# Performance work log

Measured on AMD Instinct MI355X. Metric: run time of the kernel, lower is better.

## Reference

```python
import jax, jax.numpy as jnp
import numpy as np

NEG_SLOPE = 0.2

def leaky_relu(x):
    return jnp.where(x >= 0, x, NEG_SLOPE * x)

def conv1x1(x, w, b):
    # x: [n,c,h,w], w: [o,c], b: [o]
    return jnp.einsum('nchw,oc->nohw', x, w) + b[None, :, None, None]

def setup_inputs() -> dict:
    key = jax.random.key(0)
    ks = jax.random.split(key, 7)
    n, c, h, w = 4, 64, 80, 80
    scale = 1.0 / np.sqrt(c)
    return {
        'x': jax.random.normal(ks[0], (n, c, h, w), dtype=jnp.float32),
        'w1': jax.random.normal(ks[1], (c, c), dtype=jnp.float32) * scale,
        'b1': jax.random.normal(ks[2], (c,), dtype=jnp.float32) * 0.01,
        'w2': jax.random.normal(ks[3], (c, c), dtype=jnp.float32) * scale,
        'b2': jax.random.normal(ks[4], (c,), dtype=jnp.float32) * 0.01,
        'w3': jax.random.normal(ks[5], (c, c), dtype=jnp.float32) * scale,
        'b3': jax.random.normal(ks[6], (c,), dtype=jnp.float32) * 0.01,
    }

def reference(x, w1, b1, w2, b2, w3, b3):
    n, c, h, w = x.shape
    e1 = leaky_relu(conv1x1(x, w1, b1))  # [n,c,h,w]
    e2 = leaky_relu(conv1x1(x, w2, b2))
    asm = leaky_relu(conv1x1(x, w3, b3))
    # q: [n, hw, c]; k: [n, c, hw]
    q = e1.transpose(0, 2, 3, 1).reshape(n, h * w, c)
    k = e2.reshape(n, c, h * w)
    score = jax.nn.softmax(jnp.matmul(q, k), axis=2)  # [n, hw, hw]
    v = asm.reshape(n, c, h * w).transpose(0, 2, 1)   # [n, hw, c]
    out = jnp.matmul(score, v)                        # [n, hw, c]
    return out.transpose(0, 2, 1).reshape(n, c, h, w)
```

## Files before the change

kernel.cpp:

```cpp
#include <hip/hip_runtime.h>


typedef __attribute__((ext_vector_type(8))) unsigned short us8;
typedef __attribute__((ext_vector_type(4))) unsigned short us4;
typedef __attribute__((ext_vector_type(8))) __bf16 bf16x8;
typedef __attribute__((ext_vector_type(16))) float f32x16;

#define HW 6400
#define L2E 1.44269504088896340736f
#define KS 5
#define ITERS 20

union V8 { us8 s; us4 h[2]; bf16x8 b; unsigned u4[4]; };

__device__ __forceinline__ unsigned short f32_to_bf16(float f) {
  unsigned u = __float_as_uint(f);
  u += 0x7fffu + ((u >> 16) & 1u);
  return (unsigned short)(u >> 16);
}
__device__ __forceinline__ float bf16_bits_to_f32(unsigned short u) {
  return __uint_as_float(((unsigned)u) << 16);
}
__device__ __forceinline__ unsigned pack_bf16x2(float a, float b) {
#if __has_builtin(__builtin_amdgcn_cvt_pk_bf16_f32)
  auto v = __builtin_amdgcn_cvt_pk_bf16_f32(a, b);
  unsigned u;
  __builtin_memcpy(&u, &v, 4);
  return u;
#else
  unsigned ua = __float_as_uint(a); ua += 0x7fffu + ((ua >> 16) & 1u);
  unsigned ub = __float_as_uint(b); ub += 0x7fffu + ((ub >> 16) & 1u);
  return (ua >> 16) | (ub & 0xffff0000u);
#endif
}

__global__ __launch_bounds__(256) void wprep_kernel(
    const float* __restrict__ w1, const float* __restrict__ b1,
    const float* __restrict__ w2, const float* __restrict__ w3,
    unsigned short* __restrict__ Whl, float* __restrict__ b1s) {
  const int tid = blockIdx.x * 256 + threadIdx.x;
  if (tid < 3 * 4096) {
    const int k = tid >> 12;
    const int rem = tid & 4095;
    const float* wsrc = (k == 0) ? w1 : (k == 1) ? w2 : w3;
    float v = wsrc[rem];
    if (k == 0) v *= L2E;
    const unsigned short hi = f32_to_bf16(v);
    const unsigned short lo = f32_to_bf16(v - bf16_bits_to_f32(hi));
    Whl[(size_t)(k * 2) * 4096 + rem] = hi;
    Whl[(size_t)(k * 2 + 1) * 4096 + rem] = lo;
  }
  if (tid < 64) b1s[tid] = b1[tid] * L2E;
}

__global__ __launch_bounds__(256, 2) void conv_kernel(
    const float* __restrict__ x, const unsigned short* __restrict__ Whl,
    const float* __restrict__ b1s, const float* __restrict__ b2,
    const float* __restrict__ b3,
    unsigned short* __restrict__ Qg, unsigned short* __restrict__ Kg,
    unsigned short* __restrict__ Vg) {
  __shared__ __align__(16) unsigned short Xh[64 * 72];
  __shared__ __align__(16) unsigned short Xl[64 * 72];
  __shared__ __align__(16) unsigned short tb[64 * 72];

  const int t = threadIdx.x;
  const int n = blockIdx.y;
  const int p0 = blockIdx.x * 64;
  const int wv = t >> 6;
  const int lane = t & 63;
  const int l31 = lane & 31;
  const int lh = lane >> 5;
  const int ob = (wv & 1) * 32;
  const int pw = (wv >> 1) * 32;

  {
    const int c2 = t >> 3;
    const int pg = (t & 7) * 8;
    const float* s0 = x + ((size_t)(n * 64 + 2 * c2) * HW + p0 + pg);
    const float* s1 = s0 + HW;
    float a0[8], a1[8];
    *(float4*)(a0) = *(const float4*)s0;
    *(float4*)(a0 + 4) = *(const float4*)(s0 + 4);
    *(float4*)(a1) = *(const float4*)s1;
    *(float4*)(a1 + 4) = *(const float4*)(s1 + 4);
#pragma unroll
    for (int j = 0; j < 8; ++j) {
      const unsigned hp = pack_bf16x2(a0[j], a1[j]);
      const float r0 = a0[j] - bf16_bits_to_f32((unsigned short)(hp & 0xffffu));
      const float r1 = a1[j] - bf16_bits_to_f32((unsigned short)(hp >> 16));
      const unsigned lq = pack_bf16x2(r0, r1);
      ((unsigned*)Xh)[(pg + j) * 36 + c2] = hp;
      ((unsigned*)Xl)[(pg + j) * 36 + c2] = lq;
    }
  }
  __syncthreads();

#pragma unroll 1
  for (int k = 0; k < 3; ++k) {
    const unsigned short* Wh = Whl + (size_t)(k * 2) * 4096;
    const unsigned short* Wl = Wh + 4096;
    const float* bm = (k == 0) ? b1s : (k == 1) ? b2 : b3;

    V8 ah[4], al[4];
#pragma unroll
    for (int kst = 0; kst < 4; ++kst) {
      const int off = (ob + l31) * 64 + kst * 16 + lh * 8;
      ah[kst].s = *(const us8*)(Wh + off);
      al[kst].s = *(const us8*)(Wl + off);
    }

    f32x16 acc;
#pragma unroll
    for (int r = 0; r < 16; ++r) acc[r] = 0.f;

#pragma unroll
    for (int kst = 0; kst < 4; ++kst) {
      V8 bh, bl;
      const int xoff = (pw + l31) * 72 + kst * 16 + lh * 8;
      bh.s = *(const us8*)(Xh + xoff);
      bl.s = *(const us8*)(Xl + xoff);
      acc = __builtin_amdgcn_mfma_f32_32x32x16_bf16(al[kst].b, bh.b, acc, 0, 0, 0);
      acc = __builtin_amdgcn_mfma_f32_32x32x16_bf16(ah[kst].b, bl.b, acc, 0, 0, 0);
      acc = __builtin_amdgcn_mfma_f32_32x32x16_bf16(ah[kst].b, bh.b, acc, 0, 0, 0);
    }

    if (k < 2) {
#pragma unroll
      for (int rq = 0; rq < 4; ++rq) {
        const int o = ob + 8 * rq + 4 * lh;
        const int pcol = pw + l31;
        float v[4];
#pragma unroll
        for (int j = 0; j < 4; ++j) {
          float a = acc[4 * rq + j] + bm[o + j];
          a = fmaxf(a, 0.f) + 0.2f * fminf(a, 0.f);
          v[j] = a;
        }
        unsigned* dst = (unsigned*)(tb + pcol * 72 + o);
        dst[0] = pack_bf16x2(v[0], v[1]);
        dst[1] = pack_bf16x2(v[2], v[3]);
      }
      __syncthreads();
      {
        const int p = t >> 2, part = t & 3;
        const unsigned short* src = tb + p * 72 + part * 16;
        unsigned short* dst = (k == 0 ? Qg : Kg) +
                              (size_t)(n * HW + p0 + p) * 64 + part * 16;
        *(us8*)dst = *(const us8*)src;
        *(us8*)(dst + 8) = *(const us8*)(src + 8);
      }
      __syncthreads();
    } else {
#pragma unroll
      for (int r = 0; r < 16; ++r) {
        const int o = ob + 8 * (r >> 2) + 4 * lh + (r & 3);
        const int pcol = pw + l31;
        float a = acc[r] + bm[o];
        a = fmaxf(a, 0.f) + 0.2f * fminf(a, 0.f);
        Vg[(size_t)(n * 64 + o) * HW + p0 + pcol] = f32_to_bf16(a);
      }
    }
  }
}

__global__ __launch_bounds__(256, 4) void attn_kernel(
    const unsigned short* __restrict__ Qg, const unsigned short* __restrict__ Kg,
    const unsigned short* __restrict__ Vg, unsigned short* __restrict__ Opart,
    float* __restrict__ Lpart) {
  __shared__ __align__(16) char smem[36864];
  unsigned short* Otb = (unsigned short*)smem;

  const int t = threadIdx.x;
  const int w = t >> 6;
  const int lane = t & 63;
  const int l31 = lane & 31;
  const int lh = lane >> 5;
  const int nb = blockIdx.y;
  const int qb = blockIdx.x * 128;
  const int ks = blockIdx.z;
  const int key0 = ks * (HW / KS);

  V8 aQ[4];
  {
    const unsigned short* qrow =
        Qg + (size_t)(nb * HW + qb + w * 32 + l31) * 64 + lh * 8;
#pragma unroll
    for (int kst = 0; kst < 4; ++kst) aQ[kst].s = *(const us8*)(qrow + kst * 16);
  }

  f32x16 accO[2];
#pragma unroll
  for (int ci = 0; ci < 2; ++ci)
#pragma unroll
    for (int r = 0; r < 16; ++r) accO[ci][r] = 0.f;
  float lp = 0.f;

  f32x16 zero16;
#pragma unroll
  for (int r = 0; r < 16; ++r) zero16[r] = 0.f;

  const int soff = (t >> 2) * 72 + (t & 3) * 16;
  const unsigned short* ksrc =
      Kg + (size_t)nb * HW * 64 + (size_t)(key0 + (t >> 2)) * 64 + (t & 3) * 16;
  const unsigned short* vsrc =
      Vg + (size_t)nb * 64 * HW + (size_t)(t >> 2) * HW + key0 + (t & 3) * 16;

  V8 kr0, kr1, vr0, vr1;
  kr0.s = *(const us8*)ksrc;
  kr1.s = *(const us8*)(ksrc + 8);
  vr0.s = *(const us8*)vsrc;
  vr1.s = *(const us8*)(vsrc + 8);
  {
    unsigned short* kd = (unsigned short*)smem + soff;
    unsigned short* vd = (unsigned short*)(smem + 18432) + soff;
    *(us8*)kd = kr0.s; *(us8*)(kd + 8) = kr1.s;
    *(us8*)vd = vr0.s; *(us8*)(vd + 8) = vr1.s;
  }
  __syncthreads();

#pragma unroll 1
  for (int jt = 0; jt < ITERS; ++jt) {
    const int b = jt & 1;
    const unsigned short* Kc = (const unsigned short*)(smem + b * 9216);
    const unsigned short* Vc = (const unsigned short*)(smem + 18432 + b * 9216);
    const bool more = (jt + 1 < ITERS);

    if (more) {
      kr0.s = *(const us8*)(ksrc + (jt + 1) * 4096);
      kr1.s = *(const us8*)(ksrc + (jt + 1) * 4096 + 8);
      vr0.s = *(const us8*)(vsrc + (jt + 1) * 64);
      vr1.s = *(const us8*)(vsrc + (jt + 1) * 64 + 8);
    }

#pragma unroll
    for (int ni = 0; ni < 2; ++ni) {
      V8 ak[4];
#pragma unroll
      for (int kst = 0; kst < 4; ++kst)
        ak[kst].s = *(const us8*)(Kc + (ni * 32 + l31) * 72 + kst * 16 + lh * 8);
      f32x16 sacc =
          __builtin_amdgcn_mfma_f32_32x32x16_bf16(ak[0].b, aQ[0].b, zero16, 0, 0, 0);
#pragma unroll
      for (int kst = 1; kst < 4; ++kst)
        sacc = __builtin_amdgcn_mfma_f32_32x32x16_bf16(ak[kst].b, aQ[kst].b,
                                                       sacc, 0, 0, 0);
      uint2 pkg[4];
#pragma unroll
      for (int g = 0; g < 4; ++g) {
        const float p0 = __builtin_amdgcn_exp2f(sacc[4 * g + 0]);
        const float p1 = __builtin_amdgcn_exp2f(sacc[4 * g + 1]);
        const float p2 = __builtin_amdgcn_exp2f(sacc[4 * g + 2]);
        const float p3 = __builtin_amdgcn_exp2f(sacc[4 * g + 3]);
        lp += (p0 + p1) + (p2 + p3);
        pkg[g].x = pack_bf16x2(p0, p1);
        pkg[g].y = pack_bf16x2(p2, p3);
      }

      V8 bv[2][2];
#pragma unroll
      for (int ci = 0; ci < 2; ++ci)
#pragma unroll
        for (int kk = 0; kk < 2; ++kk)
          bv[ci][kk].s = *(const us8*)(Vc + (ci * 32 + l31) * 72 +
                                       (2 * ni + kk) * 16 + lh * 8);
#pragma unroll
      for (int kk = 0; kk < 2; ++kk) {
        const int gb = 2 * kk;
        V8 ap;
#if __has_builtin(__builtin_amdgcn_permlane32_swap)
        {
          auto rx = __builtin_amdgcn_permlane32_swap(pkg[gb].x, pkg[gb + 1].x,
                                                     false, false);
          auto ry = __builtin_amdgcn_permlane32_swap(pkg[gb].y, pkg[gb + 1].y,
                                                     false, false);
          ap.u4[0] = rx[0]; ap.u4[2] = rx[1];
          ap.u4[1] = ry[0]; ap.u4[3] = ry[1];
        }
#else
        {
          const uint2 qa = pkg[gb];
          const uint2 qb2 = pkg[gb + 1];
          uint2 send;
          send.x = lh ? qa.x : qb2.x;
          send.y = lh ? qa.y : qb2.y;
          uint2 recv;
          recv.x = __shfl_xor(send.x, 32);
          recv.y = __shfl_xor(send.y, 32);
          const uint2 keep = {lh ? qb2.x : qa.x, lh ? qb2.y : qa.y};
          ap.u4[0] = lh ? recv.x : keep.x;
          ap.u4[1] = lh ? recv.y : keep.y;
          ap.u4[2] = lh ? keep.x : recv.x;
          ap.u4[3] = lh ? keep.y : recv.y;
        }
#endif
        accO[0] = __builtin_amdgcn_mfma_f32_32x32x16_bf16(ap.b, bv[0][kk].b,
                                                          accO[0], 0, 0, 0);
        accO[1] = __builtin_amdgcn_mfma_f32_32x32x16_bf16(ap.b, bv[1][kk].b,
                                                          accO[1], 0, 0, 0);
      }
    }

    if (more) {
      unsigned short* kd = (unsigned short*)(smem + (1 - b) * 9216) + soff;
      unsigned short* vd = (unsigned short*)(smem + 18432 + (1 - b) * 9216) + soff;
      *(us8*)kd = kr0.s; *(us8*)(kd + 8) = kr1.s;
      *(us8*)vd = vr0.s; *(us8*)(vd + 8) = vr1.s;
      __syncthreads();
    }
  }

  {
    const float lsum = lp + __shfl_xor(lp, 32);
    if (lh == 0)
      Lpart[((size_t)ks * 4 + nb) * HW + qb + w * 32 + l31] = lsum;
  }

  __syncthreads();
#pragma unroll
  for (int ci = 0; ci < 2; ++ci)
#pragma unroll
    for (int r = 0; r < 16; ++r) {
      const int qcol = w * 32 + 8 * (r >> 2) + 4 * lh + (r & 3);
      Otb[(ci * 32 + l31) * 132 + qcol] = f32_to_bf16(accO[ci][r]);
    }
  __syncthreads();
  {
    const int ch = t >> 2, part = t & 3;
    const unsigned short* src = Otb + ch * 132 + part * 32;
    unsigned short* dst =
        Opart + (((size_t)ks * 4 + nb) * 64 + ch) * HW + qb + part * 32;
#pragma unroll
    for (int i = 0; i < 4; ++i) {
      V8 v;
      v.h[0] = *(const us4*)(src + i * 8);
      v.h[1] = *(const us4*)(src + i * 8 + 4);
      *(us8*)(dst + i * 8) = v.s;
    }
  }
}

__global__ __launch_bounds__(256) void combine_kernel(
    const unsigned short* __restrict__ Opart, const float* __restrict__ Lpart,
    float* __restrict__ out) {
  const int tid = blockIdx.x * 256 + threadIdx.x;
  const size_t e = (size_t)tid * 4;
  float4 o = {0.f, 0.f, 0.f, 0.f};
#pragma unroll
  for (int ks = 0; ks < KS; ++ks) {
    const us4 v = *(const us4*)(Opart + (size_t)ks * (4 * 64 * HW) + e);
    o.x += bf16_bits_to_f32(v[0]);
    o.y += bf16_bits_to_f32(v[1]);
    o.z += bf16_bits_to_f32(v[2]);
    o.w += bf16_bits_to_f32(v[3]);
  }
  const int n = (int)(e / (64 * HW));
  const int p = (int)(e % HW);
  float4 l = {0.f, 0.f, 0.f, 0.f};
#pragma unroll
  for (int ks = 0; ks < KS; ++ks) {
    const float4 v = *(const float4*)(Lpart + ((size_t)ks * 4 + n) * HW + p);
    l.x += v.x; l.y += v.y; l.z += v.z; l.w += v.w;
  }
  float4 r;
  r.x = o.x / l.x; r.y = o.y / l.y; r.z = o.z / l.z; r.w = o.w / l.w;
  *(float4*)(out + e) = r;
}

extern "C" void kernel_launch(void* const* d_in, const int* in_sizes, int n_in,
                              void* d_out, int out_size, void* d_ws, size_t ws_size,
                              hipStream_t stream) {
  const float* x = (const float*)d_in[0];
  const float* w1 = (const float*)d_in[1];
  const float* b1 = (const float*)d_in[2];
  const float* w2 = (const float*)d_in[3];
  const float* b2 = (const float*)d_in[4];
  const float* w3 = (const float*)d_in[5];
  const float* b3 = (const float*)d_in[6];
  float* out = (float*)d_out;

  unsigned short* Q = (unsigned short*)d_ws;
  unsigned short* K = Q + (size_t)4 * HW * 64;
  unsigned short* V = K + (size_t)4 * HW * 64;
  unsigned short* Opart = V + (size_t)4 * HW * 64;
  float* Lpart = (float*)(Opart + (size_t)KS * 4 * 64 * HW);
  unsigned short* Whl = (unsigned short*)(Lpart + (size_t)KS * 4 * HW);
  float* b1s = (float*)(Whl + 3 * 2 * 4096);

  wprep_kernel<<<48, 256, 0, stream>>>(w1, b1, w2, w3, Whl, b1s);
  conv_kernel<<<dim3(100, 4), 256, 0, stream>>>(x, Whl, b1s, b2, b3, Q, K, V);
  attn_kernel<<<dim3(50, 4, KS), 256, 0, stream>>>(Q, K, V, Opart, Lpart);
  combine_kernel<<<1600, 256, 0, stream>>>(Opart, Lpart, out);
}
```

Before: 145.3 us.

## Fuse split-K combine into attention kernel via last-block atomic counter

Removes the separate combine kernel. Each attention block bumps a per-tile atomic counter once its partial output is written, and the last of the KS key-split blocks sums the bf16 partials and the L partials, then writes the normalized output. This saves one kernel launch and lets the combine overlap with attention blocks still running, at the cost of a threadfence and an atomic per block and a serialized reduction tail in the last block. The counters are reset inside wprep on every call.

```diff
diff --git a/kernel.cpp b/kernel.cpp
--- a/kernel.cpp
+++ b/kernel.cpp
@@ -37,7 +37,8 @@
 __global__ __launch_bounds__(256) void wprep_kernel(
     const float* __restrict__ w1, const float* __restrict__ b1,
     const float* __restrict__ w2, const float* __restrict__ w3,
-    unsigned short* __restrict__ Whl, float* __restrict__ b1s) {
+    unsigned short* __restrict__ Whl, float* __restrict__ b1s,
+    int* __restrict__ cnt) {
   const int tid = blockIdx.x * 256 + threadIdx.x;
   if (tid < 3 * 4096) {
     const int k = tid >> 12;
@@ -51,6 +52,7 @@
     Whl[(size_t)(k * 2 + 1) * 4096 + rem] = lo;
   }
   if (tid < 64) b1s[tid] = b1[tid] * L2E;
+  if (tid < 200) cnt[tid] = 0;
 }
 
 __global__ __launch_bounds__(256, 2) void conv_kernel(
@@ -166,7 +168,8 @@
 __global__ __launch_bounds__(256, 4) void attn_kernel(
     const unsigned short* __restrict__ Qg, const unsigned short* __restrict__ Kg,
     const unsigned short* __restrict__ Vg, unsigned short* __restrict__ Opart,
-    float* __restrict__ Lpart) {
+    float* __restrict__ Lpart, int* __restrict__ cnt,
+    float* __restrict__ out) {
   __shared__ __align__(16) char smem[36864];
   unsigned short* Otb = (unsigned short*)smem;
 
@@ -337,33 +340,60 @@
       *(us8*)(dst + i * 8) = v.s;
     }
   }
-}
-
-__global__ __launch_bounds__(256) void combine_kernel(
-    const unsigned short* __restrict__ Opart, const float* __restrict__ Lpart,
-    float* __restrict__ out) {
-  const int tid = blockIdx.x * 256 + threadIdx.x;
-  const size_t e = (size_t)tid * 4;
-  float4 o = {0.f, 0.f, 0.f, 0.f};
-#pragma unroll
-  for (int ks = 0; ks < KS; ++ks) {
-    const us4 v = *(const us4*)(Opart + (size_t)ks * (4 * 64 * HW) + e);
-    o.x += bf16_bits_to_f32(v[0]);
-    o.y += bf16_bits_to_f32(v[1]);
-    o.z += bf16_bits_to_f32(v[2]);
-    o.w += bf16_bits_to_f32(v[3]);
-  }
-  const int n = (int)(e / (64 * HW));
-  const int p = (int)(e % HW);
-  float4 l = {0.f, 0.f, 0.f, 0.f};
-#pragma unroll
-  for (int ks = 0; ks < KS; ++ks) {
-    const float4 v = *(const float4*)(Lpart + ((size_t)ks * 4 + n) * HW + p);
-    l.x += v.x; l.y += v.y; l.z += v.z; l.w += v.w;
-  }
-  float4 r;
-  r.x = o.x / l.x; r.y = o.y / l.y; r.z = o.z / l.z; r.w = o.w / l.w;
-  *(float4*)(out + e) = r;
+
+  __threadfence();
+  __syncthreads();
+  __shared__ int lastflag;
+  if (t == 0) {
+    const int old = __hip_atomic_fetch_add(&cnt[nb * 50 + blockIdx.x], 1,
+                                           __ATOMIC_ACQ_REL,
+                                           __HIP_MEMORY_SCOPE_AGENT);
+    lastflag = (old == KS - 1);
+  }
+  __syncthreads();
+  if (!lastflag) return;
+  __threadfence();
+
+  {
+    const int c = t >> 2;
+    const int pseg = (t & 3) * 32;
+#pragma unroll
+    for (int hhalf = 0; hhalf < 2; ++hhalf) {
+      const int pb2 = pseg + hhalf * 16;
+      float osum[16], lsum[16];
+#pragma unroll
+      for (int j = 0; j < 16; ++j) { osum[j] = 0.f; lsum[j] = 0.f; }
+#pragma unroll
+      for (int ksi = 0; ksi < KS; ++ksi) {
+        const unsigned short* op =
+            Opart + (((size_t)ksi * 4 + nb) * 64 + c) * HW + qb + pb2;
+        const us8 v0 = *(const us8*)op;
+        const us8 v1 = *(const us8*)(op + 8);
+#pragma unroll
+        for (int j = 0; j < 8; ++j) {
+          osum[j] += bf16_bits_to_f32(v0[j]);
+          osum[8 + j] += bf16_bits_to_f32(v1[j]);
+        }
+        const float* lptr = Lpart + ((size_t)ksi * 4 + nb) * HW + qb + pb2;
+#pragma unroll
+        for (int j = 0; j < 4; ++j) {
+          const float4 lv = *(const float4*)(lptr + j * 4);
+          lsum[4 * j + 0] += lv.x; lsum[4 * j + 1] += lv.y;
+          lsum[4 * j + 2] += lv.z; lsum[4 * j + 3] += lv.w;
+        }
+      }
+      float* od = out + ((size_t)nb * 64 + c) * HW + qb + pb2;
+#pragma unroll
+      for (int j = 0; j < 4; ++j) {
+        float4 r;
+        r.x = osum[4 * j + 0] / lsum[4 * j + 0];
+        r.y = osum[4 * j + 1] / lsum[4 * j + 1];
+        r.z = osum[4 * j + 2] / lsum[4 * j + 2];
+        r.w = osum[4 * j + 3] / lsum[4 * j + 3];
+        *(float4*)(od + j * 4) = r;
+      }
+    }
+  }
 }
 
 extern "C" void kernel_launch(void* const* d_in, const int* in_sizes, int n_in,
@@ -385,9 +415,10 @@
   float* Lpart = (float*)(Opart + (size_t)KS * 4 * 64 * HW);
   unsigned short* Whl = (unsigned short*)(Lpart + (size_t)KS * 4 * HW);
   float* b1s = (float*)(Whl + 3 * 2 * 4096);
-
-  wprep_kernel<<<48, 256, 0, stream>>>(w1, b1, w2, w3, Whl, b1s);
+  int* cnt = (int*)(b1s + 64);
+
+  wprep_kernel<<<48, 256, 0, stream>>>(w1, b1, w2, w3, Whl, b1s, cnt);
   conv_kernel<<<dim3(100, 4), 256, 0, stream>>>(x, Whl, b1s, b2, b3, Q, K, V);
-  attn_kernel<<<dim3(50, 4, KS), 256, 0, stream>>>(Q, K, V, Opart, Lpart);
-  combine_kernel<<<1600, 256, 0, stream>>>(Opart, Lpart, out);
-}
+  attn_kernel<<<dim3(50, 4, KS), 256, 0, stream>>>(Q, K, V, Opart, Lpart,
+                                                   cnt, out);
+}
```

New measurement: 334.0 us. 130% more time.

## Load K/V tiles directly from global into registers, drop LDS double-buffering

Applied to the files above, without the earlier changes.

Removes the shared-memory double-buffered staging of K and V tiles and their per-iteration barriers. Each wave now loads its MFMA operands straight from global memory (via L2/cache) into registers, with the loop unrolled by two. Occupancy bounds drop from 4 to 3 blocks to allow more registers. This trades fewer syncs and LDS traffic for redundant global loads, since all four waves fetch the same K/V, plus exposed global latency and reduced occupancy.

```diff
diff --git a/kernel.cpp b/kernel.cpp
--- a/kernel.cpp
+++ b/kernel.cpp
@@ -163,12 +163,11 @@
   }
 }
 
-__global__ __launch_bounds__(256, 4) void attn_kernel(
+__global__ __launch_bounds__(256, 3) void attn_kernel(
     const unsigned short* __restrict__ Qg, const unsigned short* __restrict__ Kg,
     const unsigned short* __restrict__ Vg, unsigned short* __restrict__ Opart,
     float* __restrict__ Lpart) {
-  __shared__ __align__(16) char smem[36864];
-  unsigned short* Otb = (unsigned short*)smem;
+  __shared__ __align__(16) unsigned short Otb[64 * 132];
 
   const int t = threadIdx.x;
   const int w = t >> 6;
@@ -199,45 +198,35 @@
 #pragma unroll
   for (int r = 0; r < 16; ++r) zero16[r] = 0.f;
 
-  const int soff = (t >> 2) * 72 + (t & 3) * 16;
-  const unsigned short* ksrc =
-      Kg + (size_t)nb * HW * 64 + (size_t)(key0 + (t >> 2)) * 64 + (t & 3) * 16;
-  const unsigned short* vsrc =
-      Vg + (size_t)nb * 64 * HW + (size_t)(t >> 2) * HW + key0 + (t & 3) * 16;
-
-  V8 kr0, kr1, vr0, vr1;
-  kr0.s = *(const us8*)ksrc;
-  kr1.s = *(const us8*)(ksrc + 8);
-  vr0.s = *(const us8*)vsrc;
-  vr1.s = *(const us8*)(vsrc + 8);
-  {
-    unsigned short* kd = (unsigned short*)smem + soff;
-    unsigned short* vd = (unsigned short*)(smem + 18432) + soff;
-    *(us8*)kd = kr0.s; *(us8*)(kd + 8) = kr1.s;
-    *(us8*)vd = vr0.s; *(us8*)(vd + 8) = vr1.s;
-  }
-  __syncthreads();
-
-#pragma unroll 1
+  const unsigned short* Kw = Kg + ((size_t)nb * HW + key0) * 64;
+  const unsigned short* Vw = Vg + (size_t)nb * 64 * HW + key0;
+
+#pragma unroll 2
   for (int jt = 0; jt < ITERS; ++jt) {
-    const int b = jt & 1;
-    const unsigned short* Kc = (const unsigned short*)(smem + b * 9216);
-    const unsigned short* Vc = (const unsigned short*)(smem + 18432 + b * 9216);
-    const bool more = (jt + 1 < ITERS);
-
-    if (more) {
-      kr0.s = *(const us8*)(ksrc + (jt + 1) * 4096);
-      kr1.s = *(const us8*)(ksrc + (jt + 1) * 4096 + 8);
-      vr0.s = *(const us8*)(vsrc + (jt + 1) * 64);
-      vr1.s = *(const us8*)(vsrc + (jt + 1) * 64 + 8);
-    }
+    const int kb = jt * 64;
+
+    V8 ak0[4], ak1[4];
+#pragma unroll
+    for (int kst = 0; kst < 4; ++kst) {
+      ak0[kst].s = *(const us8*)(Kw + (size_t)(kb + l31) * 64 + kst * 16 + lh * 8);
+      ak1[kst].s =
+          *(const us8*)(Kw + (size_t)(kb + 32 + l31) * 64 + kst * 16 + lh * 8);
+    }
+    V8 bv0[2][2], bv1[2][2];
+#pragma unroll
+    for (int ci = 0; ci < 2; ++ci)
+#pragma unroll
+      for (int kk = 0; kk < 2; ++kk) {
+        const unsigned short* vrow = Vw + (size_t)(ci * 32 + l31) * HW + kb;
+        bv0[ci][kk].s = *(const us8*)(vrow + kk * 16 + lh * 8);
+        bv1[ci][kk].s = *(const us8*)(vrow + 32 + kk * 16 + lh * 8);
+      }
 
 #pragma unroll
     for (int ni = 0; ni < 2; ++ni) {
-      V8 ak[4];
-#pragma unroll
-      for (int kst = 0; kst < 4; ++kst)
-        ak[kst].s = *(const us8*)(Kc + (ni * 32 + l31) * 72 + kst * 16 + lh * 8);
+      V8* ak = ni ? ak1 : ak0;
+      V8(*bv)[2] = ni ? bv1 : bv0;
+
       f32x16 sacc =
           __builtin_amdgcn_mfma_f32_32x32x16_bf16(ak[0].b, aQ[0].b, zero16, 0, 0, 0);
 #pragma unroll
@@ -256,13 +245,6 @@
         pkg[g].y = pack_bf16x2(p2, p3);
       }
 
-      V8 bv[2][2];
-#pragma unroll
-      for (int ci = 0; ci < 2; ++ci)
-#pragma unroll
-        for (int kk = 0; kk < 2; ++kk)
-          bv[ci][kk].s = *(const us8*)(Vc + (ci * 32 + l31) * 72 +
-                                       (2 * ni + kk) * 16 + lh * 8);
 #pragma unroll
       for (int kk = 0; kk < 2; ++kk) {
         const int gb = 2 * kk;
@@ -299,14 +281,6 @@
                                                           accO[1], 0, 0, 0);
       }
     }
-
-    if (more) {
-      unsigned short* kd = (unsigned short*)(smem + (1 - b) * 9216) + soff;
-      unsigned short* vd = (unsigned short*)(smem + 18432 + (1 - b) * 9216) + soff;
-      *(us8*)kd = kr0.s; *(us8*)(kd + 8) = kr1.s;
-      *(us8*)vd = vr0.s; *(us8*)(vd + 8) = vr1.s;
-      __syncthreads();
-    }
   }
 
   {
@@ -315,7 +289,6 @@
       Lpart[((size_t)ks * 4 + nb) * HW + qb + w * 32 + l31] = lsum;
   }
 
-  __syncthreads();
 #pragma unroll
   for (int ci = 0; ci < 2; ++ci)
 #pragma unroll
```

Result: slower. 245.4 us (+68.9%).

## Process two query tiles per wave to reuse K/V LDS fragments

Applied to the files above, without the earlier changes.

Each wave now handles 64 query rows (two 32-row MFMA tiles) instead of 32, so every K and V fragment loaded from shared memory feeds twice as many MFMAs. The attention grid is halved to 25x4x5 blocks and launch bounds drop to 2 blocks per CU to allow the larger register footprint. The output staging buffer is widened to a 266-element row stride. The trade-off is fewer blocks to spread over the CUs, lower occupancy, and potentially misaligned 8-byte shared loads from the new stride.

```diff
diff --git a/kernel.cpp b/kernel.cpp
--- a/kernel.cpp
+++ b/kernel.cpp
@@ -163,7 +163,7 @@
   }
 }
 
-__global__ __launch_bounds__(256, 4) void attn_kernel(
+__global__ __launch_bounds__(256, 2) void attn_kernel(
     const unsigned short* __restrict__ Qg, const unsigned short* __restrict__ Kg,
     const unsigned short* __restrict__ Vg, unsigned short* __restrict__ Opart,
     float* __restrict__ Lpart) {
@@ -176,24 +176,28 @@
   const int l31 = lane & 31;
   const int lh = lane >> 5;
   const int nb = blockIdx.y;
-  const int qb = blockIdx.x * 128;
+  const int qb = blockIdx.x * 256;
   const int ks = blockIdx.z;
   const int key0 = ks * (HW / KS);
 
-  V8 aQ[4];
-  {
+  V8 aQ[2][4];
+#pragma unroll
+  for (int h = 0; h < 2; ++h) {
     const unsigned short* qrow =
-        Qg + (size_t)(nb * HW + qb + w * 32 + l31) * 64 + lh * 8;
-#pragma unroll
-    for (int kst = 0; kst < 4; ++kst) aQ[kst].s = *(const us8*)(qrow + kst * 16);
-  }
-
-  f32x16 accO[2];
-#pragma unroll
-  for (int ci = 0; ci < 2; ++ci)
-#pragma unroll
-    for (int r = 0; r < 16; ++r) accO[ci][r] = 0.f;
-  float lp = 0.f;
+        Qg + (size_t)(nb * HW + qb + w * 64 + h * 32 + l31) * 64 + lh * 8;
+#pragma unroll
+    for (int kst = 0; kst < 4; ++kst)
+      aQ[h][kst].s = *(const us8*)(qrow + kst * 16);
+  }
+
+  f32x16 accO[2][2];
+#pragma unroll
+  for (int h = 0; h < 2; ++h)
+#pragma unroll
+    for (int ci = 0; ci < 2; ++ci)
+#pragma unroll
+      for (int r = 0; r < 16; ++r) accO[h][ci][r] = 0.f;
+  float lp0 = 0.f, lp1 = 0.f;
 
   f32x16 zero16;
 #pragma unroll
@@ -238,22 +242,29 @@
 #pragma unroll
       for (int kst = 0; kst < 4; ++kst)
         ak[kst].s = *(const us8*)(Kc + (ni * 32 + l31) * 72 + kst * 16 + lh * 8);
-      f32x16 sacc =
-          __builtin_amdgcn_mfma_f32_32x32x16_bf16(ak[0].b, aQ[0].b, zero16, 0, 0, 0);
-#pragma unroll
-      for (int kst = 1; kst < 4; ++kst)
-        sacc = __builtin_amdgcn_mfma_f32_32x32x16_bf16(ak[kst].b, aQ[kst].b,
-                                                       sacc, 0, 0, 0);
-      uint2 pkg[4];
-#pragma unroll
-      for (int g = 0; g < 4; ++g) {
-        const float p0 = __builtin_amdgcn_exp2f(sacc[4 * g + 0]);
-        const float p1 = __builtin_amdgcn_exp2f(sacc[4 * g + 1]);
-        const float p2 = __builtin_amdgcn_exp2f(sacc[4 * g + 2]);
-        const float p3 = __builtin_amdgcn_exp2f(sacc[4 * g + 3]);
-        lp += (p0 + p1) + (p2 + p3);
-        pkg[g].x = pack_bf16x2(p0, p1);
-        pkg[g].y = pack_bf16x2(p2, p3);
+
+      uint2 pkg[2][4];
+#pragma unroll
+      for (int h = 0; h < 2; ++h) {
+        f32x16 sacc = __builtin_amdgcn_mfma_f32_32x32x16_bf16(
+            ak[0].b, aQ[h][0].b, zero16, 0, 0, 0);
+#pragma unroll
+        for (int kst = 1; kst < 4; ++kst)
+          sacc = __builtin_amdgcn_mfma_f32_32x32x16_bf16(ak[kst].b,
+                                                         aQ[h][kst].b, sacc,
+                                                         0, 0, 0);
+        float lps = 0.f;
+#pragma unroll
+        for (int g = 0; g < 4; ++g) {
+          const float p0 = __builtin_amdgcn_exp2f(sacc[4 * g + 0]);
+          const float p1 = __builtin_amdgcn_exp2f(sacc[4 * g + 1]);
+          const float p2 = __builtin_amdgcn_exp2f(sacc[4 * g + 2]);
+          const float p3 = __builtin_amdgcn_exp2f(sacc[4 * g + 3]);
+          lps += (p0 + p1) + (p2 + p3);
+          pkg[h][g].x = pack_bf16x2(p0, p1);
+          pkg[h][g].y = pack_bf16x2(p2, p3);
+        }
+        if (h == 0) lp0 += lps; else lp1 += lps;
       }
 
       V8 bv[2][2];
@@ -263,40 +274,44 @@
         for (int kk = 0; kk < 2; ++kk)
           bv[ci][kk].s = *(const us8*)(Vc + (ci * 32 + l31) * 72 +
                                        (2 * ni + kk) * 16 + lh * 8);
+
 #pragma unroll
       for (int kk = 0; kk < 2; ++kk) {
         const int gb = 2 * kk;
-        V8 ap;
+#pragma unroll
+        for (int h = 0; h < 2; ++h) {
+          V8 ap;
 #if __has_builtin(__builtin_amdgcn_permlane32_swap)
-        {
-          auto rx = __builtin_amdgcn_permlane32_swap(pkg[gb].x, pkg[gb + 1].x,
-                                                     false, false);
-          auto ry = __builtin_amdgcn_permlane32_swap(pkg[gb].y, pkg[gb + 1].y,
-                                                     false, false);
-          ap.u4[0] = rx[0]; ap.u4[2] = rx[1];
-          ap.u4[1] = ry[0]; ap.u4[3] = ry[1];
+          {
+            auto rx = __builtin_amdgcn_permlane32_swap(
+                pkg[h][gb].x, pkg[h][gb + 1].x, false, false);
+            auto ry = __builtin_amdgcn_permlane32_swap(
+                pkg[h][gb].y, pkg[h][gb + 1].y, false, false);
+            ap.u4[0] = rx[0]; ap.u4[2] = rx[1];
+            ap.u4[1] = ry[0]; ap.u4[3] = ry[1];
+          }
+#else
+          {
+            const uint2 qa = pkg[h][gb];
+            const uint2 qb2 = pkg[h][gb + 1];
+            uint2 send;
+            send.x = lh ? qa.x : qb2.x;
+            send.y = lh ? qa.y : qb2.y;
+            uint2 recv;
+            recv.x = __shfl_xor(send.x, 32);
+            recv.y = __shfl_xor(send.y, 32);
+            const uint2 keep = {lh ? qb2.x : qa.x, lh ? qb2.y : qa.y};
+            ap.u4[0] = lh ? recv.x : keep.x;
+            ap.u4[1] = lh ? recv.y : keep.y;
+            ap.u4[2] = lh ? keep.x : recv.x;
+            ap.u4[3] = lh ? keep.y : recv.y;
+          }
+#endif
+          accO[h][0] = __builtin_amdgcn_mfma_f32_32x32x16_bf16(
+              ap.b, bv[0][kk].b, accO[h][0], 0, 0, 0);
+          accO[h][1] = __builtin_amdgcn_mfma_f32_32x32x16_bf16(
+              ap.b, bv[1][kk].b, accO[h][1], 0, 0, 0);
         }
-#else
-        {
-          const uint2 qa = pkg[gb];
-          const uint2 qb2 = pkg[gb + 1];
-          uint2 send;
-          send.x = lh ? qa.x : qb2.x;
-          send.y = lh ? qa.y : qb2.y;
-          uint2 recv;
-          recv.x = __shfl_xor(send.x, 32);
-          recv.y = __shfl_xor(send.y, 32);
-          const uint2 keep = {lh ? qb2.x : qa.x, lh ? qb2.y : qa.y};
-          ap.u4[0] = lh ? recv.x : keep.x;
-          ap.u4[1] = lh ? recv.y : keep.y;
-          ap.u4[2] = lh ? keep.x : recv.x;
-          ap.u4[3] = lh ? keep.y : recv.y;
-        }
-#endif
-        accO[0] = __builtin_amdgcn_mfma_f32_32x32x16_bf16(ap.b, bv[0][kk].b,
-                                                          accO[0], 0, 0, 0);
-        accO[1] = __builtin_amdgcn_mfma_f32_32x32x16_bf16(ap.b, bv[1][kk].b,
-                                                          accO[1], 0, 0, 0);
       }
     }
 
@@ -310,27 +325,33 @@
   }
 
   {
-    const float lsum = lp + __shfl_xor(lp, 32);
-    if (lh == 0)
-      Lpart[((size_t)ks * 4 + nb) * HW + qb + w * 32 + l31] = lsum;
+    const float ls0 = lp0 + __shfl_xor(lp0, 32);
+    const float ls1 = lp1 + __shfl_xor(lp1, 32);
+    if (lh == 0) {
+      float* lrow = Lpart + ((size_t)ks * 4 + nb) * HW + qb + w * 64;
+      lrow[l31] = ls0;
+      lrow[32 + l31] = ls1;
+    }
   }
 
   __syncthreads();
 #pragma unroll
-  for (int ci = 0; ci < 2; ++ci)
-#pragma unroll
-    for (int r = 0; r < 16; ++r) {
-      const int qcol = w * 32 + 8 * (r >> 2) + 4 * lh + (r & 3);
-      Otb[(ci * 32 + l31) * 132 + qcol] = f32_to_bf16(accO[ci][r]);
-    }
+  for (int h = 0; h < 2; ++h)
+#pragma unroll
+    for (int ci = 0; ci < 2; ++ci)
+#pragma unroll
+      for (int r = 0; r < 16; ++r) {
+        const int qcol = w * 64 + h * 32 + 8 * (r >> 2) + 4 * lh + (r & 3);
+        Otb[(ci * 32 + l31) * 266 + qcol] = f32_to_bf16(accO[h][ci][r]);
+      }
   __syncthreads();
   {
     const int ch = t >> 2, part = t & 3;
-    const unsigned short* src = Otb + ch * 132 + part * 32;
+    const unsigned short* src = Otb + ch * 266 + part * 64;
     unsigned short* dst =
-        Opart + (((size_t)ks * 4 + nb) * 64 + ch) * HW + qb + part * 32;
-#pragma unroll
-    for (int i = 0; i < 4; ++i) {
+        Opart + (((size_t)ks * 4 + nb) * 64 + ch) * HW + qb + part * 64;
+#pragma unroll
+    for (int i = 0; i < 8; ++i) {
       V8 v;
       v.h[0] = *(const us4*)(src + i * 8);
       v.h[1] = *(const us4*)(src + i * 8 + 4);
@@ -388,6 +409,6 @@
 
   wprep_kernel<<<48, 256, 0, stream>>>(w1, b1, w2, w3, Whl, b1s);
   conv_kernel<<<dim3(100, 4), 256, 0, stream>>>(x, Whl, b1s, b2, b3, Q, K, V);
-  attn_kernel<<<dim3(50, 4, KS), 256, 0, stream>>>(Q, K, V, Opart, Lpart);
+  attn_kernel<<<dim3(25, 4, KS), 256, 0, stream>>>(Q, K, V, Opart, Lpart);
   combine_kernel<<<1600, 256, 0, stream>>>(Opart, Lpart, out);
 }
```

New measurement: 144.0 us. About the same (-0.9%).
